# Performance work log

Hardware: AMD Instinct MI355X
Metric: run time of the kernel (lower is better)

Reference implementation:

```python
import jax, jax.numpy as jnp
import numpy as np

B, N, C, K = 8, 4096, 128, 16
EPS = 1e-5  # BatchNorm1d default eps


def setup_inputs() -> dict:
    key = jax.random.key(0)
    k0, k1, k2 = jax.random.split(key, 3)
    xyz = jax.random.normal(k0, (B, N, 3), jnp.float32)
    x = jax.random.normal(k1, (B, C, N), jnp.float32)
    # Conv1d(channel, channel, kernel_size=1, bias=False) weight -> [C_out, C_in]
    W = jax.random.normal(k2, (C, C), jnp.float32) / np.sqrt(C)
    gamma = jnp.ones((C,), jnp.float32)
    beta = jnp.zeros((C,), jnp.float32)
    running_mean = jnp.zeros((C,), jnp.float32)
    running_var = jnp.ones((C,), jnp.float32)
    return {"xyz": xyz, "x": x, "W": W, "gamma": gamma, "beta": beta,
            "running_mean": running_mean, "running_var": running_var}


def _knn_idx(xyz, k):
    # squared pairwise distances d2[b,i,j] = ||xyz[b,i]-xyz[b,j]||^2
    s = jnp.sum(xyz * xyz, axis=-1)                      # [B,N]
    d2 = s[:, :, None] + s[:, None, :] - 2.0 * jnp.einsum('bnd,bmd->bnm', xyz, xyz)
    # keops argKmin over dim=1; d2 is symmetric so top_k over the last axis is equivalent
    _, idx = jax.lax.top_k(-d2, k)                       # [B,N,K]
    return idx


def reference(xyz, x, W, gamma, beta, running_mean, running_var):
    idx = _knn_idx(xyz, K)                               # [B,N,K] int32
    x_t = jnp.transpose(x, (0, 2, 1))                    # [B,N,C]
    grouped = jax.vmap(lambda pts, i: pts[i])(x_t, idx)  # [B,N,K,C] gather
    g = jnp.transpose(grouped, (0, 3, 2, 1))             # [B,C,K,N]
    # 1x1 Conv1d (no bias): GEMM over channel dim
    y = jnp.einsum('oc,bckn->bokn', W, g)                # [B,C,K,N]
    # BatchNorm1d (inference form with running stats)
    scale = gamma * jax.lax.rsqrt(running_var + EPS)     # [C]
    y = y * scale[None, :, None, None] + (beta - running_mean * scale)[None, :, None, None]
    y = jax.nn.relu(y)
    return jnp.max(y, axis=2)                            # max over k neighbors -> [B,C,N]
```

## Files before the change

### kernel.cpp

```cpp
#include <hip/hip_runtime.h>
#include <hip/hip_bf16.h>

#define BATCH 8
#define NPTS  4096
#define CCH   128
#define KNN_K 16

typedef __attribute__((ext_vector_type(8))) short  bf16x8;
typedef __attribute__((ext_vector_type(4))) float  f32x4;


static __device__ __forceinline__ short f2bf(float v) {
    __hip_bfloat16 h = __float2bfloat16(v);
    return __builtin_bit_cast(short, h);
}

__global__ __launch_bounds__(256) void transpose_kernel(
    const float* __restrict__ x, short* __restrict__ xTb)
{
    __shared__ short tile[64 * 66];
    const int tid = threadIdx.x;
    const int b   = blockIdx.x >> 7;
    const int rem = blockIdx.x & 127;
    const int nt  = rem >> 1;
    const int ct  = rem & 1;

    #pragma unroll
    for (int it = 0; it < 16; ++it) {
        const int idx = it * 256 + tid;
        const int cc  = idx >> 6;
        const int nn  = idx & 63;
        const float v = x[(size_t)(b * CCH + ct * 64 + cc) * NPTS + nt * 64 + nn];
        tile[cc * 66 + nn] = f2bf(v);
    }
    __syncthreads();
    #pragma unroll
    for (int it = 0; it < 16; ++it) {
        const int idx = it * 256 + tid;
        const int nn  = idx >> 6;
        const int cc  = idx & 63;
        xTb[(size_t)(b * NPTS + nt * 64 + nn) * CCH + ct * 64 + cc] = tile[cc * 66 + nn];
    }
}

__global__ __launch_bounds__(256) void small_prep_kernel(
    const float* __restrict__ xyz, const float* __restrict__ W,
    const float* __restrict__ gamma, const float* __restrict__ beta,
    const float* __restrict__ rmean, const float* __restrict__ rvar,
    short* __restrict__ Wb, float* __restrict__ scale, float* __restrict__ bias,
    float4* __restrict__ pts)
{
    const int t = blockIdx.x * 256 + threadIdx.x;
    if (t < CCH * CCH) Wb[t] = f2bf(W[t]);
    if (t < CCH) {
        const float s = gamma[t] / sqrtf(rvar[t] + 1e-5f);
        scale[t] = s;
        bias[t]  = beta[t] - rmean[t] * s;
    }
    {
        #pragma clang fp contract(off)
        const float px = xyz[3 * t + 0];
        const float py = xyz[3 * t + 1];
        const float pz = xyz[3 * t + 2];
        const float s  = px * px + py * py + pz * pz;
        pts[t] = make_float4(px, py, pz, s);
    }
}

#define PK_(h, l) ((((unsigned long long)(h)) << 32) | (unsigned long long)(l))

__global__ __launch_bounds__(256) void knn_kernel(
    const float4* __restrict__ pts, unsigned short* __restrict__ knn)
{
    const int lane = threadIdx.x & 63;
    const int wid  = threadIdx.x >> 6;
    const int g    = lane >> 4;
    const int s    = lane & 15;
    const int wq   = blockIdx.x * 16 + wid * 4;
    const int b    = wq >> 12;
    const int i    = (wq & 4095) + g;
    const float4* pb = pts + (b << 12);

    const float4 q = pb[i];

    const unsigned SENT_HI = 0xFF7FFFFFu;
    const unsigned SENT_LO = 0xFFFFFFFFu;

    unsigned lhi = SENT_HI, llo = SENT_LO;
    float bufD = 0.f;
    int   bufJ = 0;
    int   cnt  = 0;
    float tau  = 3.4e38f;
    const int gsh = g << 4;

    auto flush = [&]() {
        const unsigned u = __float_as_uint(bufD);
        unsigned khi = (u & 0x80000000u) ? ~u : (u | 0x80000000u);
        unsigned klo = (unsigned)bufJ;
        const bool inval = (s >= cnt);
        khi = inval ? SENT_HI : khi;
        klo = inval ? SENT_LO : klo;
        #define CE_(K, J, OFF) { \
            const unsigned ohi = (unsigned)__builtin_amdgcn_ds_swizzle((int)khi, OFF); \
            const unsigned olo = (unsigned)__builtin_amdgcn_ds_swizzle((int)klo, OFF); \
            const bool olt = PK_(ohi, olo) < PK_(khi, klo); \
            const bool sel = (((s & (J)) == 0) == ((s & (K)) == 0)); \
            const bool tk  = sel ? olt : !olt; \
            khi = tk ? ohi : khi; klo = tk ? olo : klo; }
        CE_(2, 1, 0x041F)
        CE_(4, 2, 0x081F)  CE_(4, 1, 0x041F)
        CE_(8, 4, 0x101F)  CE_(8, 2, 0x081F)  CE_(8, 1, 0x041F)
        CE_(16, 8, 0x201F) CE_(16, 4, 0x101F) CE_(16, 2, 0x081F) CE_(16, 1, 0x041F)
        #undef CE_
        {
            const unsigned rhi = (unsigned)__builtin_amdgcn_ds_swizzle((int)khi, 0x3C1F);
            const unsigned rlo = (unsigned)__builtin_amdgcn_ds_swizzle((int)klo, 0x3C1F);
            const bool rlt = PK_(rhi, rlo) < PK_(lhi, llo);
            lhi = rlt ? rhi : lhi; llo = rlt ? rlo : llo;
        }
        #define MC_(J, OFF) { \
            const unsigned ohi = (unsigned)__builtin_amdgcn_ds_swizzle((int)lhi, OFF); \
            const unsigned olo = (unsigned)__builtin_amdgcn_ds_swizzle((int)llo, OFF); \
            const bool olt = PK_(ohi, olo) < PK_(lhi, llo); \
            const bool tk  = ((s & (J)) == 0) ? olt : !olt; \
            lhi = tk ? ohi : lhi; llo = tk ? olo : llo; }
        MC_(8, 0x201F) MC_(4, 0x101F) MC_(2, 0x081F) MC_(1, 0x041F)
        #undef MC_
        const unsigned thi = (unsigned)__builtin_amdgcn_ds_swizzle((int)lhi, 0x01F0);
        tau = __uint_as_float((thi & 0x80000000u) ? (thi & 0x7FFFFFFFu) : ~thi);
        cnt = 0;
    };

    #define SUB_(DD, C, JB) { \
        const unsigned long long mask = __ballot((DD) < tau); \
        if (mask) { \
            const unsigned sub = (unsigned)((mask >> gsh) & 0xFFFFull); \
            const int m = __popc(sub); \
            if (__any(cnt + m > 15)) flush(); \
            const bool surv = (sub >> s) & 1u; \
            const int rank  = __popc(sub & ((1u << s) - 1u)); \
            const int dest  = surv ? (cnt + rank) : 15;    \
            const int addr  = (gsh | dest) << 2; \
            const int nd = __builtin_amdgcn_ds_permute(addr, __float_as_int(DD)); \
            const int nj = __builtin_amdgcn_ds_permute(addr, (JB) + ((C) << 4) + s); \
            const bool got = (s >= cnt) & (s < cnt + m); \
            bufD = got ? __int_as_float(nd) : bufD; \
            bufJ = got ? nj : bufJ; \
            cnt += m; \
        } }

    const float4* lp = pb + s;
    float4 a0 = lp[0], a1 = lp[16], a2 = lp[32], a3 = lp[48];
    lp += 64;

    #pragma unroll 1
    for (int it = 0; it < 64; ++it) {
        const float4* np = (it < 63) ? lp : pb;
        const float4 n0 = np[0], n1 = np[16], n2 = np[32], n3 = np[48];
        float dd0, dd1, dd2, dd3;
        {
            #pragma clang fp contract(off)
            dd0 = (q.w + a0.w) - 2.0f * (q.x * a0.x + q.y * a0.y + q.z * a0.z);
            dd1 = (q.w + a1.w) - 2.0f * (q.x * a1.x + q.y * a1.y + q.z * a1.z);
            dd2 = (q.w + a2.w) - 2.0f * (q.x * a2.x + q.y * a2.y + q.z * a2.z);
            dd3 = (q.w + a3.w) - 2.0f * (q.x * a3.x + q.y * a3.y + q.z * a3.z);
        }
        const int jbase = it * 64;
        SUB_(dd0, 0, jbase)
        SUB_(dd1, 1, jbase)
        SUB_(dd2, 2, jbase)
        SUB_(dd3, 3, jbase)
        a0 = n0; a1 = n1; a2 = n2; a3 = n3;
        lp += 64;
    }
    #undef SUB_
    flush();

    unsigned short* o = knn + ((((size_t)b << 12) + i) << 4);
    o[s] = (unsigned short)llo;
}

__global__ __launch_bounds__(256) void zgemm_kernel(
    const short* __restrict__ xTb, const short* __restrict__ Wb,
    short* __restrict__ Zb)
{
    __shared__ short sW[CCH * 136];
    const int lane = threadIdx.x & 63;
    const int wid  = threadIdx.x >> 6;
    const int kl   = lane & 15;
    const int q8   = (lane >> 4) * 8;

    #pragma unroll
    for (int it = 0; it < 8; ++it) {
        const int e = (it * 256 + threadIdx.x) * 8;
        const int r = e >> 7, c = e & 127;
        *(bf16x8*)(sW + r * 136 + c) = *(const bf16x8*)(Wb + e);
    }

    const int    G    = blockIdx.x * 64 + wid * 16 + kl;
    const size_t arow = (size_t)G * CCH;
    __syncthreads();

    const f32x4 zero = {0.f, 0.f, 0.f, 0.f};
    f32x4 acc[8];
    #pragma unroll
    for (int t = 0; t < 8; ++t) acc[t] = zero;

    #pragma unroll
    for (int kk = 0; kk < 4; ++kk) {
        const bf16x8 a = *(const bf16x8*)(xTb + arow + kk * 32 + q8);
        #pragma unroll
        for (int t = 0; t < 8; ++t) {
            const bf16x8 bf = *(const bf16x8*)(sW + (t * 16 + kl) * 136 + kk * 32 + q8);
            acc[t] = __builtin_amdgcn_mfma_f32_16x16x32_bf16(a, bf, acc[t], 0, 0, 0);
        }
    }

    const int rbase = blockIdx.x * 64 + wid * 16 + (lane >> 4) * 4;
    #pragma unroll
    for (int t = 0; t < 8; ++t)
        #pragma unroll
        for (int r = 0; r < 4; ++r)
            Zb[(size_t)(rbase + r) * CCH + t * 16 + kl] = f2bf(acc[t][r]);
}

__global__ __launch_bounds__(256) void gmax_kernel(
    const short* __restrict__ Zb, const unsigned short* __restrict__ knn,
    const float* __restrict__ scale, const float* __restrict__ bias,
    float* __restrict__ out)
{
    __shared__ float sm[16][132];
    const int lane = threadIdx.x & 63;
    const int wid  = threadIdx.x >> 6;
    const int n0   = blockIdx.x * 16;
    const int b    = blockIdx.x >> 8;
    const float s0 = scale[2 * lane],   s1 = scale[2 * lane + 1];
    const float t0 = bias[2 * lane],    t1 = bias[2 * lane + 1];

    for (int p = 0; p < 4; ++p) {
        const int n = n0 + wid * 4 + p;
        const unsigned short* kr = knn + (size_t)n * 16;
        float m0 = 0.f, m1 = 0.f;
        #pragma unroll
        for (int k = 0; k < 16; ++k) {
            const int r = (int)kr[k];
            const unsigned v = *(const unsigned*)(Zb + ((size_t)(b * NPTS + r)) * CCH + 2 * lane);
            const float z0 = __uint_as_float(v << 16);
            const float z1 = __uint_as_float(v & 0xFFFF0000u);
            m0 = fmaxf(m0, s0 * z0 + t0);
            m1 = fmaxf(m1, s1 * z1 + t1);
        }
        sm[wid * 4 + p][2 * lane]     = m0;
        sm[wid * 4 + p][2 * lane + 1] = m1;
    }
    __syncthreads();

    const int c    = threadIdx.x & 127;
    const int half = threadIdx.x >> 7;
    float v[8];
    #pragma unroll
    for (int i = 0; i < 8; ++i) v[i] = sm[half * 8 + i][c];
    float4 f0 = {v[0], v[1], v[2], v[3]};
    float4 f1 = {v[4], v[5], v[6], v[7]};
    float* op = out + ((size_t)(b * CCH + c)) * NPTS + (n0 & 4095) + half * 8;
    *(float4*)op       = f0;
    *(float4*)(op + 4) = f1;
}

extern "C" void kernel_launch(void* const* d_in, const int* in_sizes, int n_in,
                              void* d_out, int out_size, void* d_ws, size_t ws_size,
                              hipStream_t stream)
{
    const float* xyz   = (const float*)d_in[0];
    const float* x     = (const float*)d_in[1];
    const float* W     = (const float*)d_in[2];
    const float* gamma = (const float*)d_in[3];
    const float* beta  = (const float*)d_in[4];
    const float* rmean = (const float*)d_in[5];
    const float* rvar  = (const float*)d_in[6];
    float* out = (float*)d_out;

    char* ws = (char*)d_ws;
    short*          xTb   = (short*)(ws);
    short*          Wb    = (short*)(ws + 8388608);
    float*          scale = (float*)(ws + 8421376);
    float*          bias  = (float*)(ws + 8421888);
    float4*         pts   = (float4*)(ws + 8422400);
    unsigned short* knn   = (unsigned short*)(ws + 8946688);
    short*          Zb    = (short*)(ws + 9995264);

    transpose_kernel<<<BATCH * 64 * 2, 256, 0, stream>>>(x, xTb);
    small_prep_kernel<<<BATCH * NPTS / 256, 256, 0, stream>>>(
        xyz, W, gamma, beta, rmean, rvar, Wb, scale, bias, pts);
    knn_kernel<<<BATCH * NPTS / 16, 256, 0, stream>>>(pts, knn);
    zgemm_kernel<<<BATCH * NPTS / 64, 256, 0, stream>>>(xTb, Wb, Zb);
    gmax_kernel<<<BATCH * NPTS / 16, 256, 0, stream>>>(Zb, knn, scale, bias, out);
}
```

Baseline: 116.7 us.

## Fuse KNN and Z-GEMM into one interleaved launch and seed KNN threshold early

The KNN and Z-GEMM kernels are merged into a single launch in which every fifth block runs the GEMM body and the other four run KNN, so the memory- and MFMA-bound GEMM work overlaps the compare-heavy KNN work and one launch disappears. The GEMM drops its LDS staging of W and reads W straight from global memory, with loops partly rolled to cut register pressure under the new launch bound of 8 blocks. KNN now seeds its top-16 list by sorting the first 16 candidates and sets the threshold immediately, which lets later candidates be rejected earlier. It also double-buffers the point loads with an explicit two-stage prefetch. The risks are lower occupancy when the two bodies share one register budget and W reads that now go through global memory and cache instead of LDS.

Result: slower. 120.6 us (+3.3%).

```diff
diff --git a/kernel.cpp b/kernel.cpp
--- a/kernel.cpp
+++ b/kernel.cpp
@@ -69,14 +69,15 @@
 
 #define PK_(h, l) ((((unsigned long long)(h)) << 32) | (unsigned long long)(l))
 
-__global__ __launch_bounds__(256) void knn_kernel(
+static __device__ __forceinline__ void knn_body(
+    const int bid, const int tid,
     const float4* __restrict__ pts, unsigned short* __restrict__ knn)
 {
-    const int lane = threadIdx.x & 63;
-    const int wid  = threadIdx.x >> 6;
+    const int lane = tid & 63;
+    const int wid  = tid >> 6;
     const int g    = lane >> 4;
     const int s    = lane & 15;
-    const int wq   = blockIdx.x * 16 + wid * 4;
+    const int wq   = bid * 16 + wid * 4;
     const int b    = wq >> 12;
     const int i    = (wq & 4095) + g;
     const float4* pb = pts + (b << 12);
@@ -92,6 +93,26 @@
     int   cnt  = 0;
     float tau  = 3.4e38f;
     const int gsh = g << 4;
+
+    auto sort16 = [&](unsigned& hi, unsigned& lo) {
+        #define CE_(K, J, OFF) { \
+            const unsigned ohi = (unsigned)__builtin_amdgcn_ds_swizzle((int)hi, OFF); \
+            const unsigned olo = (unsigned)__builtin_amdgcn_ds_swizzle((int)lo, OFF); \
+            const bool olt = PK_(ohi, olo) < PK_(hi, lo); \
+            const bool sel = (((s & (J)) == 0) == ((s & (K)) == 0)); \
+            const bool tk  = sel ? olt : !olt; \
+            hi = tk ? ohi : hi; lo = tk ? olo : lo; }
+        CE_(2, 1, 0x041F)
+        CE_(4, 2, 0x081F)  CE_(4, 1, 0x041F)
+        CE_(8, 4, 0x101F)  CE_(8, 2, 0x081F)  CE_(8, 1, 0x041F)
+        CE_(16, 8, 0x201F) CE_(16, 4, 0x101F) CE_(16, 2, 0x081F) CE_(16, 1, 0x041F)
+        #undef CE_
+    };
+
+    auto refresh_tau = [&]() {
+        const unsigned thi = (unsigned)__builtin_amdgcn_ds_swizzle((int)lhi, 0x01F0);
+        tau = __uint_as_float((thi & 0x80000000u) ? (thi & 0x7FFFFFFFu) : ~thi);
+    };
 
     auto flush = [&]() {
         const unsigned u = __float_as_uint(bufD);
@@ -100,18 +121,7 @@
         const bool inval = (s >= cnt);
         khi = inval ? SENT_HI : khi;
         klo = inval ? SENT_LO : klo;
-        #define CE_(K, J, OFF) { \
-            const unsigned ohi = (unsigned)__builtin_amdgcn_ds_swizzle((int)khi, OFF); \
-            const unsigned olo = (unsigned)__builtin_amdgcn_ds_swizzle((int)klo, OFF); \
-            const bool olt = PK_(ohi, olo) < PK_(khi, klo); \
-            const bool sel = (((s & (J)) == 0) == ((s & (K)) == 0)); \
-            const bool tk  = sel ? olt : !olt; \
-            khi = tk ? ohi : khi; klo = tk ? olo : klo; }
-        CE_(2, 1, 0x041F)
-        CE_(4, 2, 0x081F)  CE_(4, 1, 0x041F)
-        CE_(8, 4, 0x101F)  CE_(8, 2, 0x081F)  CE_(8, 1, 0x041F)
-        CE_(16, 8, 0x201F) CE_(16, 4, 0x101F) CE_(16, 2, 0x081F) CE_(16, 1, 0x041F)
-        #undef CE_
+        sort16(khi, klo);
         {
             const unsigned rhi = (unsigned)__builtin_amdgcn_ds_swizzle((int)khi, 0x3C1F);
             const unsigned rlo = (unsigned)__builtin_amdgcn_ds_swizzle((int)klo, 0x3C1F);
@@ -126,8 +136,7 @@
             lhi = tk ? ohi : lhi; llo = tk ? olo : llo; }
         MC_(8, 0x201F) MC_(4, 0x101F) MC_(2, 0x081F) MC_(1, 0x041F)
         #undef MC_
-        const unsigned thi = (unsigned)__builtin_amdgcn_ds_swizzle((int)lhi, 0x01F0);
-        tau = __uint_as_float((thi & 0x80000000u) ? (thi & 0x7FFFFFFFu) : ~thi);
+        refresh_tau();
         cnt = 0;
     };
 
@@ -149,14 +158,27 @@
             cnt += m; \
         } }
 
+    auto process = [&](const float4& p0, const float4& p1,
+                       const float4& p2, const float4& p3, const int jbase) {
+        float dd0, dd1, dd2, dd3;
+        {
+            #pragma clang fp contract(off)
+            dd0 = (q.w + p0.w) - 2.0f * (q.x * p0.x + q.y * p0.y + q.z * p0.z);
+            dd1 = (q.w + p1.w) - 2.0f * (q.x * p1.x + q.y * p1.y + q.z * p1.z);
+            dd2 = (q.w + p2.w) - 2.0f * (q.x * p2.x + q.y * p2.y + q.z * p2.z);
+            dd3 = (q.w + p3.w) - 2.0f * (q.x * p3.x + q.y * p3.y + q.z * p3.z);
+        }
+        SUB_(dd0, 0, jbase)
+        SUB_(dd1, 1, jbase)
+        SUB_(dd2, 2, jbase)
+        SUB_(dd3, 3, jbase)
+    };
+
     const float4* lp = pb + s;
-    float4 a0 = lp[0], a1 = lp[16], a2 = lp[32], a3 = lp[48];
-    lp += 64;
-
-    #pragma unroll 1
-    for (int it = 0; it < 64; ++it) {
-        const float4* np = (it < 63) ? lp : pb;
-        const float4 n0 = np[0], n1 = np[16], n2 = np[32], n3 = np[48];
+    float4 a0 = lp[0],  a1 = lp[16],  a2 = lp[32],  a3 = lp[48];
+    float4 c0 = lp[64], c1 = lp[80],  c2 = lp[96],  c3 = lp[112];
+
+    {
         float dd0, dd1, dd2, dd3;
         {
             #pragma clang fp contract(off)
@@ -165,63 +187,84 @@
             dd2 = (q.w + a2.w) - 2.0f * (q.x * a2.x + q.y * a2.y + q.z * a2.z);
             dd3 = (q.w + a3.w) - 2.0f * (q.x * a3.x + q.y * a3.y + q.z * a3.z);
         }
-        const int jbase = it * 64;
-        SUB_(dd0, 0, jbase)
-        SUB_(dd1, 1, jbase)
-        SUB_(dd2, 2, jbase)
-        SUB_(dd3, 3, jbase)
-        a0 = n0; a1 = n1; a2 = n2; a3 = n3;
-        lp += 64;
-    }
+        const unsigned u = __float_as_uint(dd0);
+        lhi = (u & 0x80000000u) ? ~u : (u | 0x80000000u);
+        llo = (unsigned)s;
+        sort16(lhi, llo);
+        refresh_tau();
+        SUB_(dd1, 1, 0)
+        SUB_(dd2, 2, 0)
+        SUB_(dd3, 3, 0)
+    }
+
+    #pragma unroll 1
+    for (int t = 0; t < 31; ++t) {
+        const int blk = 1 + 2 * t;
+        const float4* p2 = lp + (blk + 1) * 64;
+        a0 = p2[0]; a1 = p2[16]; a2 = p2[32]; a3 = p2[48];
+        process(c0, c1, c2, c3, blk * 64);
+        const float4* p3 = lp + (blk + 2) * 64;
+        c0 = p3[0]; c1 = p3[16]; c2 = p3[32]; c3 = p3[48];
+        process(a0, a1, a2, a3, (blk + 1) * 64);
+    }
+    process(c0, c1, c2, c3, 63 * 64);
     #undef SUB_
+
     flush();
 
     unsigned short* o = knn + ((((size_t)b << 12) + i) << 4);
     o[s] = (unsigned short)llo;
 }
 
-__global__ __launch_bounds__(256) void zgemm_kernel(
+static __device__ __forceinline__ void zgemm_body(
+    const int bid, const int tid,
     const short* __restrict__ xTb, const short* __restrict__ Wb,
     short* __restrict__ Zb)
 {
-    __shared__ short sW[CCH * 136];
-    const int lane = threadIdx.x & 63;
-    const int wid  = threadIdx.x >> 6;
+    const int lane = tid & 63;
+    const int wid  = tid >> 6;
     const int kl   = lane & 15;
     const int q8   = (lane >> 4) * 8;
 
-    #pragma unroll
-    for (int it = 0; it < 8; ++it) {
-        const int e = (it * 256 + threadIdx.x) * 8;
-        const int r = e >> 7, c = e & 127;
-        *(bf16x8*)(sW + r * 136 + c) = *(const bf16x8*)(Wb + e);
-    }
-
-    const int    G    = blockIdx.x * 64 + wid * 16 + kl;
+    const int    G    = bid * 64 + wid * 16 + kl;
     const size_t arow = (size_t)G * CCH;
-    __syncthreads();
 
     const f32x4 zero = {0.f, 0.f, 0.f, 0.f};
     f32x4 acc[8];
     #pragma unroll
     for (int t = 0; t < 8; ++t) acc[t] = zero;
 
-    #pragma unroll
+    #pragma unroll 1
     for (int kk = 0; kk < 4; ++kk) {
         const bf16x8 a = *(const bf16x8*)(xTb + arow + kk * 32 + q8);
-        #pragma unroll
+        #pragma unroll 2
         for (int t = 0; t < 8; ++t) {
-            const bf16x8 bf = *(const bf16x8*)(sW + (t * 16 + kl) * 136 + kk * 32 + q8);
+            const bf16x8 bf = *(const bf16x8*)(Wb + (t * 16 + kl) * CCH + kk * 32 + q8);
             acc[t] = __builtin_amdgcn_mfma_f32_16x16x32_bf16(a, bf, acc[t], 0, 0, 0);
         }
     }
 
-    const int rbase = blockIdx.x * 64 + wid * 16 + (lane >> 4) * 4;
+    const int rbase = bid * 64 + wid * 16 + (lane >> 4) * 4;
     #pragma unroll
     for (int t = 0; t < 8; ++t)
         #pragma unroll
         for (int r = 0; r < 4; ++r)
             Zb[(size_t)(rbase + r) * CCH + t * 16 + kl] = f2bf(acc[t][r]);
+}
+
+__global__ __launch_bounds__(256, 8) void knn_zgemm_kernel(
+    const float4* __restrict__ pts, unsigned short* __restrict__ knn,
+    const short* __restrict__ xTb, const short* __restrict__ Wb,
+    short* __restrict__ Zb)
+{
+    const int bid = blockIdx.x;
+    const int qd  = bid / 5;
+    const int rm  = bid - qd * 5;
+    if (rm == 4) {
+        zgemm_body(qd, threadIdx.x, xTb, Wb, Zb);
+    } else {
+        knn_body(qd * 4 + rm, threadIdx.x, pts, knn);
+    }
 }
 
 __global__ __launch_bounds__(256) void gmax_kernel(
@@ -292,7 +335,7 @@
     transpose_kernel<<<BATCH * 64 * 2, 256, 0, stream>>>(x, xTb);
     small_prep_kernel<<<BATCH * NPTS / 256, 256, 0, stream>>>(
         xyz, W, gamma, beta, rmean, rvar, Wb, scale, bias, pts);
-    knn_kernel<<<BATCH * NPTS / 16, 256, 0, stream>>>(pts, knn);
-    zgemm_kernel<<<BATCH * NPTS / 64, 256, 0, stream>>>(xTb, Wb, Zb);
+    knn_zgemm_kernel<<<BATCH * NPTS / 16 + BATCH * NPTS / 64, 256, 0, stream>>>(
+        pts, knn, xTb, Wb, Zb);
     gmax_kernel<<<BATCH * NPTS / 16, 256, 0, stream>>>(Zb, knn, scale, bias, out);
 }
```
